# Optimization experiments

Measured on AMD Instinct MI355X. Metric: run time of the kernel, lower is better.

Reference implementation:

```python
import jax, jax.numpy as jnp
import numpy as np

N, E, G = 100000, 1600000, 512
D_IN, D_H, D_OUT = 128, 128, 1
EPS = 1e-5


def _gcn_conv(x, W, b, src, dst, n):
    # PyG GCNConv: h = x @ W, add self-loops, symmetric-normalized sum aggregation, bias after.
    h = x @ W
    loop = jnp.arange(n)
    s = jnp.concatenate([src, loop])
    d = jnp.concatenate([dst, loop])
    deg = jax.ops.segment_sum(jnp.ones(s.shape[0], dtype=h.dtype), d, num_segments=n)
    dinv = jnp.where(deg > 0, jax.lax.rsqrt(deg), 0.0)
    norm = dinv[s] * dinv[d]  # [E+N]
    out = jax.ops.segment_sum(h[s] * norm[:, None], d, num_segments=n)
    return out + b


def _bn(x, g, b, m, v):
    # eval-mode BatchNorm1d
    return (x - m) * jax.lax.rsqrt(v + EPS) * g + b


def setup_inputs() -> dict:
    key = jax.random.key(0)
    ks = jax.random.split(key, 24)
    x = jax.random.normal(ks[0], (N, D_IN), dtype=jnp.float32)
    edge_index = jax.random.randint(ks[1], (2, E), 0, N, dtype=jnp.int64)
    batch = (jnp.arange(N, dtype=jnp.int64) * G) // N  # sorted, all graphs non-empty
    inp = {"x": x, "edge_index": edge_index, "batch": batch}
    dims = [(D_IN, D_H), (D_H, D_H), (D_H, D_H)]
    for i, (din, dout) in enumerate(dims):
        sc = 1.0 / np.sqrt(din)
        inp[f"W{i}"] = jax.random.normal(ks[2 + 4 * i], (din, dout), dtype=jnp.float32) * sc
        inp[f"cb{i}"] = jnp.zeros((dout,), dtype=jnp.float32)
        inp[f"g{i}"] = jnp.ones((dout,), dtype=jnp.float32)
        inp[f"bt{i}"] = jnp.zeros((dout,), dtype=jnp.float32)
        inp[f"m{i}"] = jax.random.normal(ks[3 + 4 * i], (dout,), dtype=jnp.float32) * 0.1
        inp[f"v{i}"] = jax.random.uniform(ks[4 + 4 * i], (dout,), dtype=jnp.float32, minval=0.5, maxval=1.5)
    inp["L1w"] = jax.random.normal(ks[15], (2 * D_H, D_H), dtype=jnp.float32) / np.sqrt(2 * D_H)
    inp["L1b"] = jnp.zeros((D_H,), dtype=jnp.float32)
    inp["L2w"] = jax.random.normal(ks[16], (D_H, D_H // 2), dtype=jnp.float32) / np.sqrt(D_H)
    inp["L2b"] = jnp.zeros((D_H // 2,), dtype=jnp.float32)
    inp["L3w"] = jax.random.normal(ks[17], (D_H // 2, D_OUT), dtype=jnp.float32) / np.sqrt(D_H // 2)
    inp["L3b"] = jnp.zeros((D_OUT,), dtype=jnp.float32)
    return inp


def reference(x, edge_index, batch,
              W0, cb0, g0, bt0, m0, v0,
              W1, cb1, g1, bt1, m1, v1,
              W2, cb2, g2, bt2, m2, v2,
              L1w, L1b, L2w, L2b, L3w, L3b):
    src, dst = edge_index[0], edge_index[1]
    Ws = [W0, W1, W2]
    cbs = [cb0, cb1, cb2]
    bns = [(g0, bt0, m0, v0), (g1, bt1, m1, v1), (g2, bt2, m2, v2)]
    for i in range(3):
        x_prev = x
        x = _gcn_conv(x, Ws[i], cbs[i], src, dst, N)
        x = jax.nn.relu(_bn(x, *bns[i]))
        # dropout is identity in eval mode
        if i > 0:
            x = x + x_prev  # residual (shapes match for i > 0)
    ones = jnp.ones((N,), dtype=x.dtype)
    cnt = jax.ops.segment_sum(ones, batch, num_segments=G)[:, None]
    x_mean = jax.ops.segment_sum(x, batch, num_segments=G) / cnt
    x_max = jax.ops.segment_max(x, batch, num_segments=G)
    h = jnp.concatenate([x_mean, x_max], axis=1)  # [G, 2*D_H]
    h = jax.nn.relu(h @ L1w + L1b)
    h = jax.nn.relu(h @ L2w + L2b)
    return h @ L3w + L3b  # [G, 1]
```

## Files before the change

kernel.cpp:

```cpp
#include <hip/hip_runtime.h>
#include <math.h>

#define DH 128
#define EPSB 1e-5f
#define MAXB 832
#define BCAP 3072

typedef __attribute__((ext_vector_type(8))) short short8;
typedef __attribute__((ext_vector_type(4))) float f32x4;

static __device__ __forceinline__ unsigned short f2bf(float f) {
    unsigned u = __float_as_uint(f);
    u += 0x7fffu + ((u >> 16) & 1u);
    return (unsigned short)(u >> 16);
}
static __device__ __forceinline__ float bf2f(unsigned short h) {
    return __uint_as_float(((unsigned)h) << 16);
}
static __device__ __forceinline__ float blo(unsigned u) { return __uint_as_float(u << 16); }
static __device__ __forceinline__ float bhi(unsigned u) { return __uint_as_float(u & 0xFFFF0000u); }


__launch_bounds__(256)
__global__ void k_bucketA(const int* __restrict__ src, const int* __restrict__ dst,
                          int* __restrict__ gcur, int* __restrict__ bbuf,
                          const int* __restrict__ batch, int* __restrict__ starts,
                          int E, int NB, int chunk, int N, int G)
{
    __shared__ int cnt[MAXB];
    __shared__ int base[MAXB];
    const int t = threadIdx.x;

    for (int i = blockIdx.x * 256 + t; i < N; i += gridDim.x * 256) {
        int b = batch[i];
        if (i == 0) { starts[0] = 0; starts[G] = N; }
        else if (batch[i - 1] != b) starts[b] = i;
    }

    for (int i = t; i < NB; i += 256) cnt[i] = 0;
    __syncthreads();
    const int e0 = blockIdx.x * chunk;
    const int e1 = min(E, e0 + chunk);
    for (int e = e0 + t; e < e1; e += 256)
        atomicAdd(&cnt[dst[e] >> 7], 1);
    __syncthreads();
    for (int i = t; i < NB; i += 256) {
        int c = cnt[i];
        base[i] = (c > 0) ? atomicAdd(&gcur[i], c) : 0;
        cnt[i] = 0;
    }
    __syncthreads();
    for (int e = e0 + t; e < e1; e += 256) {
        int d = dst[e];
        int b = d >> 7;
        int o = base[b] + atomicAdd(&cnt[b], 1);
        if (o < BCAP) bbuf[(size_t)b * BCAP + o] = (src[e] << 7) | (d & 127);
    }
}

__launch_bounds__(1024)
__global__ void k_bgscan(const int* __restrict__ gcur, int* __restrict__ bbase,
                         int* __restrict__ rowptr, int NB, int N, int E)
{
    __shared__ int s[1024];
    int t = threadIdx.x;
    int v = (t < NB) ? min(gcur[t], BCAP) : 0;
    s[t] = v;
    __syncthreads();
    for (int off = 1; off < 1024; off <<= 1) {
        int u = (t >= off) ? s[t - off] : 0;
        __syncthreads();
        s[t] += u;
        __syncthreads();
    }
    if (t < NB) bbase[t] = s[t] - v;
    if (t == 0) rowptr[N] = E;
}

__launch_bounds__(256)
__global__ void k_bfinal(const int* __restrict__ gcur, const int* __restrict__ bbase,
                         const int* __restrict__ bbuf, int* __restrict__ rowptr,
                         float* __restrict__ dinv, int* __restrict__ csr_src, int N)
{
    __shared__ int ebuf[BCAP];
    __shared__ int dcnt[128];
    __shared__ int sp[128];
    const int b = blockIdx.x, t = threadIdx.x;
    const int c = min(gcur[b], BCAP);
    const int base = bbase[b];
    const int* p = bbuf + (size_t)b * BCAP;
    for (int i = t; i < c; i += 256) ebuf[i] = p[i];
    if (t < 128) dcnt[t] = 0;
    __syncthreads();
    for (int i = t; i < c; i += 256) atomicAdd(&dcnt[ebuf[i] & 127], 1);
    __syncthreads();
    if (t < 128) sp[t] = dcnt[t];
    __syncthreads();
    for (int off = 1; off < 128; off <<= 1) {
        int u = (t < 128 && t >= off) ? sp[t - off] : 0;
        __syncthreads();
        if (t < 128) sp[t] += u;
        __syncthreads();
    }
    if (t < 128) {
        sp[t] -= dcnt[t];
        int d = b * 128 + t;
        if (d < N) {
            rowptr[d] = base + sp[t];
            dinv[d] = rsqrtf((float)(dcnt[t] + 1));
        }
        dcnt[t] = 0;
    }
    __syncthreads();
    for (int i = t; i < c; i += 256) {
        int e = ebuf[i];
        int dl = e & 127;
        int o = atomicAdd(&dcnt[dl], 1);
        csr_src[base + sp[dl] + o] = e >> 7;
    }
}


__global__ void k_wfrag(const float* __restrict__ W0, const float* __restrict__ W1,
                        const float* __restrict__ W2, unsigned short* __restrict__ Wf0) {
    int fid = blockIdx.x * 4 + (threadIdx.x >> 6);
    int lane = threadIdx.x & 63;
    int l = fid >> 6;
    int f = fid & 63;
    const float* W = (l == 0) ? W0 : (l == 1) ? W1 : W2;
    unsigned short* Wf = Wf0 + (size_t)l * 32768;
    int nt = f & 3, s = (f >> 2) & 3, p = (f >> 4) & 1, nh = f >> 5;
    int n = nh * 64 + nt * 16 + (lane & 15);
    int kbase = s * 32 + (lane >> 4) * 8;
    unsigned short o[8];
#pragma unroll
    for (int j = 0; j < 8; ++j) {
        float w = W[(size_t)(kbase + j) * DH + n];
        unsigned short h = f2bf(w);
        o[j] = p ? f2bf(w - bf2f(h)) : h;
    }
    unsigned short* d = Wf + (size_t)f * 512 + lane * 8;
    *(ushort4*)d       = make_ushort4(o[0], o[1], o[2], o[3]);
    *(ushort4*)(d + 4) = make_ushort4(o[4], o[5], o[6], o[7]);
}


#define LDA0 132

__launch_bounds__(256)
__global__ void k_gemm0(const float* __restrict__ X,
                        const unsigned short* __restrict__ Wf,
                        const float* __restrict__ dinv,
                        unsigned short* __restrict__ hs, int N)
{
    __shared__ float As[64 * LDA0];

    const int tid  = threadIdx.x;
    const int lane = tid & 63, wave = tid >> 6;
    const int mh = wave >> 1, nh = wave & 1;
    const int rowBase = blockIdx.x * 64;
    const int r15 = lane & 15, quad = lane >> 4;

    {
        const float4* gp = (const float4*)(X + (size_t)rowBase * DH);
#pragma unroll
        for (int it = 0; it < 8; ++it) {
            int idx = it * 256 + tid;
            int grow = idx >> 5, gcol = idx & 31;
            float4 v = make_float4(0.f, 0.f, 0.f, 0.f);
            if (rowBase + grow < N) v = gp[idx];
            *(float4*)(As + grow * LDA0 + gcol * 4) = v;
        }
    }
    __syncthreads();

    f32x4 acc[2][4];
#pragma unroll
    for (int mt = 0; mt < 2; ++mt)
#pragma unroll
        for (int nt = 0; nt < 4; ++nt)
            acc[mt][nt] = (f32x4){0.f, 0.f, 0.f, 0.f};

#pragma unroll
    for (int s = 0; s < 4; ++s) {
        short8 wfh[4], wfl[4];
#pragma unroll
        for (int nt = 0; nt < 4; ++nt) {
            wfh[nt] = *(const short8*)(Wf + ((((nh * 2 + 0) * 4 + s) * 4 + nt) * 512) + lane * 8);
            wfl[nt] = *(const short8*)(Wf + ((((nh * 2 + 1) * 4 + s) * 4 + nt) * 512) + lane * 8);
        }
#pragma unroll
        for (int mt = 0; mt < 2; ++mt) {
            const float* ap = As + (mh * 32 + mt * 16 + r15) * LDA0 + s * 32 + quad * 8;
            short8 ah, al;
#pragma unroll
            for (int j = 0; j < 8; ++j) {
                float v = ap[j];
                unsigned short h = f2bf(v);
                ah[j] = (short)h;
                al[j] = (short)f2bf(v - bf2f(h));
            }
#pragma unroll
            for (int nt = 0; nt < 4; ++nt) {
                acc[mt][nt] = __builtin_amdgcn_mfma_f32_16x16x32_bf16(ah, wfh[nt], acc[mt][nt], 0, 0, 0);
                acc[mt][nt] = __builtin_amdgcn_mfma_f32_16x16x32_bf16(ah, wfl[nt], acc[mt][nt], 0, 0, 0);
                acc[mt][nt] = __builtin_amdgcn_mfma_f32_16x16x32_bf16(al, wfh[nt], acc[mt][nt], 0, 0, 0);
            }
        }
    }

#pragma unroll
    for (int mt = 0; mt < 2; ++mt) {
        int rl = mh * 32 + mt * 16 + quad * 4;
#pragma unroll
        for (int reg = 0; reg < 4; ++reg) {
            int row = rowBase + rl + reg;
            if (row < N) {
                float sc = dinv[row];
#pragma unroll
                for (int nt = 0; nt < 4; ++nt)
                    hs[(size_t)row * DH + nh * 64 + nt * 16 + r15] = f2bf(acc[mt][nt][reg] * sc);
            }
        }
    }
}


#define LDAP 136

__launch_bounds__(256)
__global__ void k_gemm_pl(const unsigned short* __restrict__ Xh,
                          const unsigned short* __restrict__ Xl,
                          const unsigned short* __restrict__ Wf,
                          const float* __restrict__ dinv,
                          unsigned short* __restrict__ hs, int N)
{
    __shared__ unsigned short Ah[64 * LDAP];
    __shared__ unsigned short Al[64 * LDAP];

    const int tid  = threadIdx.x;
    const int lane = tid & 63, wave = tid >> 6;
    const int mh = wave >> 1, nh = wave & 1;
    const int rowBase = blockIdx.x * 64;
    const int r15 = lane & 15, quad = lane >> 4;

    {
        const uint4* gh = (const uint4*)(Xh + (size_t)rowBase * DH);
        const uint4* gl = (const uint4*)(Xl + (size_t)rowBase * DH);
#pragma unroll
        for (int it = 0; it < 4; ++it) {
            int idx = it * 256 + tid;
            int grow = idx >> 4, gcol8 = (idx & 15) * 8;
            uint4 vh = make_uint4(0, 0, 0, 0), vl = make_uint4(0, 0, 0, 0);
            if (rowBase + grow < N) { vh = gh[idx]; vl = gl[idx]; }
            *(uint4*)(Ah + grow * LDAP + gcol8) = vh;
            *(uint4*)(Al + grow * LDAP + gcol8) = vl;
        }
    }
    __syncthreads();

    f32x4 acc[2][4];
#pragma unroll
    for (int mt = 0; mt < 2; ++mt)
#pragma unroll
        for (int nt = 0; nt < 4; ++nt)
            acc[mt][nt] = (f32x4){0.f, 0.f, 0.f, 0.f};

#pragma unroll
    for (int s = 0; s < 4; ++s) {
        short8 wfh[4], wfl[4];
#pragma unroll
        for (int nt = 0; nt < 4; ++nt) {
            wfh[nt] = *(const short8*)(Wf + ((((nh * 2 + 0) * 4 + s) * 4 + nt) * 512) + lane * 8);
            wfl[nt] = *(const short8*)(Wf + ((((nh * 2 + 1) * 4 + s) * 4 + nt) * 512) + lane * 8);
        }
#pragma unroll
        for (int mt = 0; mt < 2; ++mt) {
            int arow = mh * 32 + mt * 16 + r15;
            short8 ah = *(const short8*)(Ah + arow * LDAP + s * 32 + quad * 8);
            short8 al = *(const short8*)(Al + arow * LDAP + s * 32 + quad * 8);
#pragma unroll
            for (int nt = 0; nt < 4; ++nt) {
                acc[mt][nt] = __builtin_amdgcn_mfma_f32_16x16x32_bf16(ah, wfh[nt], acc[mt][nt], 0, 0, 0);
                acc[mt][nt] = __builtin_amdgcn_mfma_f32_16x16x32_bf16(ah, wfl[nt], acc[mt][nt], 0, 0, 0);
                acc[mt][nt] = __builtin_amdgcn_mfma_f32_16x16x32_bf16(al, wfh[nt], acc[mt][nt], 0, 0, 0);
            }
        }
    }

#pragma unroll
    for (int mt = 0; mt < 2; ++mt) {
        int rl = mh * 32 + mt * 16 + quad * 4;
#pragma unroll
        for (int reg = 0; reg < 4; ++reg) {
            int row = rowBase + rl + reg;
            if (row < N) {
                float sc = dinv[row];
#pragma unroll
                for (int nt = 0; nt < 4; ++nt)
                    hs[(size_t)row * DH + nh * 64 + nt * 16 + r15] = f2bf(acc[mt][nt][reg] * sc);
            }
        }
    }
}


__launch_bounds__(256)
__global__ void k_gather(const unsigned short* __restrict__ hs, const int* __restrict__ rowptr,
                         const int* __restrict__ csr_src, const float* __restrict__ dinv,
                         const float* __restrict__ cb, const float* __restrict__ bm,
                         const float* __restrict__ bv, const float* __restrict__ bg,
                         const float* __restrict__ bb,
                         const unsigned short* __restrict__ ph,
                         const unsigned short* __restrict__ pl,
                         unsigned short* __restrict__ oh,
                         unsigned short* __restrict__ ol,
                         int N)
{
    const int node = (blockIdx.x * blockDim.x + threadIdx.x) >> 4;
    const int lh = threadIdx.x & 15;
    if (node >= N) return;
    const int f = lh * 8;
    const int e0 = rowptr[node], e1 = rowptr[node + 1];

    const uint4* hsv = (const uint4*)hs;
    float a[8];
    {
        uint4 sv = hsv[(size_t)node * 16 + lh];
        a[0] = blo(sv.x); a[1] = bhi(sv.x); a[2] = blo(sv.y); a[3] = bhi(sv.y);
        a[4] = blo(sv.z); a[5] = bhi(sv.z); a[6] = blo(sv.w); a[7] = bhi(sv.w);
    }

    for (int base = e0; base < e1; base += 16) {
        int cnt = e1 - base; if (cnt > 16) cnt = 16;
        int idx = (lh < cnt) ? csr_src[base + lh] : 0;
        int i = 0;
        for (; i + 4 <= cnt; i += 4) {
            int s0 = __shfl(idx, i,     16), s1 = __shfl(idx, i + 1, 16);
            int s2 = __shfl(idx, i + 2, 16), s3 = __shfl(idx, i + 3, 16);
            uint4 v0 = hsv[(size_t)s0 * 16 + lh];
            uint4 v1 = hsv[(size_t)s1 * 16 + lh];
            uint4 v2 = hsv[(size_t)s2 * 16 + lh];
            uint4 v3 = hsv[(size_t)s3 * 16 + lh];
            a[0] += (blo(v0.x) + blo(v1.x)) + (blo(v2.x) + blo(v3.x));
            a[1] += (bhi(v0.x) + bhi(v1.x)) + (bhi(v2.x) + bhi(v3.x));
            a[2] += (blo(v0.y) + blo(v1.y)) + (blo(v2.y) + blo(v3.y));
            a[3] += (bhi(v0.y) + bhi(v1.y)) + (bhi(v2.y) + bhi(v3.y));
            a[4] += (blo(v0.z) + blo(v1.z)) + (blo(v2.z) + blo(v3.z));
            a[5] += (bhi(v0.z) + bhi(v1.z)) + (bhi(v2.z) + bhi(v3.z));
            a[6] += (blo(v0.w) + blo(v1.w)) + (blo(v2.w) + blo(v3.w));
            a[7] += (bhi(v0.w) + bhi(v1.w)) + (bhi(v2.w) + bhi(v3.w));
        }
        for (; i < cnt; ++i) {
            int s = __shfl(idx, i, 16);
            uint4 v = hsv[(size_t)s * 16 + lh];
            a[0] += blo(v.x); a[1] += bhi(v.x); a[2] += blo(v.y); a[3] += bhi(v.y);
            a[4] += blo(v.z); a[5] += bhi(v.z); a[6] += blo(v.w); a[7] += bhi(v.w);
        }
    }

    const float sc = dinv[node];
    float cbv[8], bmv[8], bvv[8], bgv[8], bbv[8];
    *(float4*)cbv = *(const float4*)(cb + f); *(float4*)(cbv + 4) = *(const float4*)(cb + f + 4);
    *(float4*)bmv = *(const float4*)(bm + f); *(float4*)(bmv + 4) = *(const float4*)(bm + f + 4);
    *(float4*)bvv = *(const float4*)(bv + f); *(float4*)(bvv + 4) = *(const float4*)(bv + f + 4);
    *(float4*)bgv = *(const float4*)(bg + f); *(float4*)(bgv + 4) = *(const float4*)(bg + f + 4);
    *(float4*)bbv = *(const float4*)(bb + f); *(float4*)(bbv + 4) = *(const float4*)(bb + f + 4);

    float o[8];
#pragma unroll
    for (int j = 0; j < 8; ++j) {
        float v = (a[j] * sc + cbv[j] - bmv[j]) * rsqrtf(bvv[j] + EPSB) * bgv[j] + bbv[j];
        o[j] = fmaxf(v, 0.f);
    }
    if (ph) {
        uint4 hv = *(const uint4*)(ph + (size_t)node * DH + f);
        uint4 lv = *(const uint4*)(pl + (size_t)node * DH + f);
        o[0] += blo(hv.x) + blo(lv.x); o[1] += bhi(hv.x) + bhi(lv.x);
        o[2] += blo(hv.y) + blo(lv.y); o[3] += bhi(hv.y) + bhi(lv.y);
        o[4] += blo(hv.z) + blo(lv.z); o[5] += bhi(hv.z) + bhi(lv.z);
        o[6] += blo(hv.w) + blo(lv.w); o[7] += bhi(hv.w) + bhi(lv.w);
    }
    unsigned hw[4], lw[4];
#pragma unroll
    for (int p = 0; p < 4; ++p) {
        unsigned short hA = f2bf(o[2 * p]), hB = f2bf(o[2 * p + 1]);
        hw[p] = (unsigned)hA | ((unsigned)hB << 16);
        lw[p] = (unsigned)f2bf(o[2 * p] - bf2f(hA)) |
                ((unsigned)f2bf(o[2 * p + 1] - bf2f(hB)) << 16);
    }
    *(uint4*)(oh + (size_t)node * DH + f) = make_uint4(hw[0], hw[1], hw[2], hw[3]);
    *(uint4*)(ol + (size_t)node * DH + f) = make_uint4(lw[0], lw[1], lw[2], lw[3]);
}


__launch_bounds__(256)
__global__ void k_pool_mlp(const unsigned short* __restrict__ xh,
                           const unsigned short* __restrict__ xl,
                           const int* __restrict__ starts,
                           const float* __restrict__ L1w, const float* __restrict__ L1b,
                           const float* __restrict__ L2w, const float* __restrict__ L2b,
                           const float* __restrict__ L3w, const float* __restrict__ L3b,
                           float* __restrict__ out)
{
    int g = blockIdx.x, t = threadIdx.x;
    int s0 = starts[g], s1 = starts[g + 1];
    const int rg = t >> 6;
    const int tc = t & 63;
    const int fc = tc * 2;

    float sA = 0.f, sB = 0.f;
    float mA = -INFINITY, mB = -INFINITY;
    for (int i = s0 + rg; i < s1; i += 4) {
        unsigned hv = *(const unsigned*)(xh + (size_t)i * DH + fc);
        unsigned lv = *(const unsigned*)(xl + (size_t)i * DH + fc);
        float vA = blo(hv) + blo(lv);
        float vB = bhi(hv) + bhi(lv);
        sA += vA; sB += vB;
        mA = fmaxf(mA, vA); mB = fmaxf(mB, vB);
    }

    __shared__ float ps[4][128];
    __shared__ float pm[4][128];
    ps[rg][fc] = sA; ps[rg][fc + 1] = sB;
    pm[rg][fc] = mA; pm[rg][fc + 1] = mB;
    __syncthreads();

    __shared__ float h[256];
    if (rg == 0) {
        float inv = 1.f / (float)(s1 - s0);
#pragma unroll
        for (int j = 0; j < 2; ++j) {
            int fi = fc + j;
            h[fi] = ((ps[0][fi] + ps[1][fi]) + (ps[2][fi] + ps[3][fi])) * inv;
            h[128 + fi] = fmaxf(fmaxf(pm[0][fi], pm[1][fi]), fmaxf(pm[2][fi], pm[3][fi]));
        }
    }
    __syncthreads();

    __shared__ float h1[128];
    if (t < 128) {
        float a = L1b[t];
        for (int k = 0; k < 256; ++k) a += h[k] * L1w[k * DH + t];
        h1[t] = fmaxf(a, 0.f);
    }
    __syncthreads();

    __shared__ float h2[64];
    if (t < 64) {
        float a2 = L2b[t];
        for (int k = 0; k < 128; ++k) a2 += h1[k] * L2w[k * 64 + t];
        h2[t] = fmaxf(a2, 0.f);
    }
    __syncthreads();

    if (t < 64) {
        float p = h2[t] * L3w[t];
#pragma unroll
        for (int off = 32; off > 0; off >>= 1) p += __shfl_down(p, off, 64);
        if (t == 0) out[g] = p + L3b[0];
    }
}


static inline char* align16(char* p) {
    return (char*)(((uintptr_t)p + 15) & ~(uintptr_t)15);
}

extern "C" void kernel_launch(void* const* d_in, const int* in_sizes, int n_in,
                              void* d_out, int out_size, void* d_ws, size_t ws_size,
                              hipStream_t stream)
{
    const float* x     = (const float*)d_in[0];
    const int*   ei    = (const int*)d_in[1];
    const int*   batch = (const int*)d_in[2];
    const int N = in_sizes[0] / DH;
    const int E = in_sizes[1] / 2;
    const int G = out_size;
    const int* src = ei;
    const int* dst = ei + E;

    const float* W[3]  = {(const float*)d_in[3],  (const float*)d_in[9],  (const float*)d_in[15]};
    const float* cb[3] = {(const float*)d_in[4],  (const float*)d_in[10], (const float*)d_in[16]};
    const float* bg[3] = {(const float*)d_in[5],  (const float*)d_in[11], (const float*)d_in[17]};
    const float* bt[3] = {(const float*)d_in[6],  (const float*)d_in[12], (const float*)d_in[18]};
    const float* bm[3] = {(const float*)d_in[7],  (const float*)d_in[13], (const float*)d_in[19]};
    const float* bv[3] = {(const float*)d_in[8],  (const float*)d_in[14], (const float*)d_in[20]};
    const float* L1w = (const float*)d_in[21]; const float* L1b = (const float*)d_in[22];
    const float* L2w = (const float*)d_in[23]; const float* L2b = (const float*)d_in[24];
    const float* L3w = (const float*)d_in[25]; const float* L3b = (const float*)d_in[26];

    char* wsp = (char*)d_ws;
    size_t planeB = (size_t)N * DH * sizeof(unsigned short);
    unsigned short* HS  = (unsigned short*)wsp; wsp += planeB;
    unsigned short* AH  = (unsigned short*)wsp; wsp += planeB;
    unsigned short* AL  = (unsigned short*)wsp; wsp += planeB;
    unsigned short* BH  = (unsigned short*)wsp; wsp += planeB;
    unsigned short* BL  = (unsigned short*)wsp; wsp += planeB;
    unsigned short* Wfrag = (unsigned short*)wsp; wsp += 3 * 65536;
    float* dinv   = (float*)wsp; wsp += (size_t)N * sizeof(float);
    int*   rowptr = (int*)wsp;   wsp = align16(wsp + (size_t)(N + 1) * sizeof(int));
    int*   csr_src= (int*)wsp;   wsp += (size_t)E * sizeof(int);
    int*   starts = (int*)wsp;   wsp = align16(wsp + (size_t)(G + 1) * sizeof(int));
    int*   gcur   = (int*)wsp;   wsp = align16(wsp + (size_t)MAXB * sizeof(int));
    int*   bbase  = (int*)wsp;   wsp = align16(wsp + (size_t)MAXB * sizeof(int));
    int*   bbuf   = (int*)wsp;   wsp += (size_t)MAXB * BCAP * sizeof(int);

    const int NB = (N + 127) >> 7;
    const int nblkA = 512;
    const int chunk = (E + nblkA - 1) / nblkA;

    hipMemsetAsync(gcur, 0, (size_t)NB * sizeof(int), stream);
    k_bucketA<<<nblkA, 256, 0, stream>>>(src, dst, gcur, bbuf, batch, starts,
                                         E, NB, chunk, N, G);
    k_bgscan <<<1, 1024, 0, stream>>>(gcur, bbase, rowptr, NB, N, E);
    k_bfinal <<<NB, 256, 0, stream>>>(gcur, bbase, bbuf, rowptr, dinv, csr_src, N);
    k_wfrag  <<<48, 256, 0, stream>>>(W[0], W[1], W[2], Wfrag);

    int gemmGrid = (N + 63) / 64;
    int gathGrid = ((size_t)N * 16 + 255) / 256;

    k_gemm0<<<gemmGrid, 256, 0, stream>>>(x, Wfrag, dinv, HS, N);
    k_gather<<<gathGrid, 256, 0, stream>>>(HS, rowptr, csr_src, dinv,
                                           cb[0], bm[0], bv[0], bg[0], bt[0],
                                           nullptr, nullptr, AH, AL, N);
    k_gemm_pl<<<gemmGrid, 256, 0, stream>>>(AH, AL, Wfrag + 32768, dinv, HS, N);
    k_gather<<<gathGrid, 256, 0, stream>>>(HS, rowptr, csr_src, dinv,
                                           cb[1], bm[1], bv[1], bg[1], bt[1],
                                           AH, AL, BH, BL, N);
    k_gemm_pl<<<gemmGrid, 256, 0, stream>>>(BH, BL, Wfrag + 65536, dinv, HS, N);
    k_gather<<<gathGrid, 256, 0, stream>>>(HS, rowptr, csr_src, dinv,
                                           cb[2], bm[2], bv[2], bg[2], bt[2],
                                           BH, BL, AH, AL, N);

    k_pool_mlp<<<G, 256, 0, stream>>>(AH, AL, starts, L1w, L1b, L2w, L2b, L3w, L3b,
                                      (float*)d_out);
}
```

Measured before the change: 507.4 us.

## Fuse neighbor gather with next-layer GEMM and drop CSR scan kernel

Each layer's gather/BN/ReLU/residual step now also runs the next layer's bf16 split-precision MFMA GEMM on its 16-node tile held in shared memory. This removes the separate GEMM kernels and the hi/lo bf16 activation planes, which are replaced by fp32 feature buffers. The CSR is built in place inside the padded per-bucket buffers, with int2 row ranges, so the global scan kernel is gone. The weight-fragment packing is folded into the bucketing launch as extra blocks. The trade-offs are a small GEMM tile per block with repeated weight-fragment loads, more fp32 feature traffic, and a smaller bucket capacity that could overflow on skewed degree distributions.

```diff
diff --git a/kernel.cpp b/kernel.cpp
--- a/kernel.cpp
+++ b/kernel.cpp
@@ -4,7 +4,8 @@
 #define DH 128
 #define EPSB 1e-5f
 #define MAXB 832
-#define BCAP 3072
+#define BCAP 2560
+#define LDAP 136
 
 typedef __attribute__((ext_vector_type(8))) short short8;
 typedef __attribute__((ext_vector_type(4))) float f32x4;
@@ -25,13 +26,38 @@
 __global__ void k_bucketA(const int* __restrict__ src, const int* __restrict__ dst,
                           int* __restrict__ gcur, int* __restrict__ bbuf,
                           const int* __restrict__ batch, int* __restrict__ starts,
+                          const float* __restrict__ W0, const float* __restrict__ W1,
+                          const float* __restrict__ W2, unsigned short* __restrict__ Wf0,
                           int E, int NB, int chunk, int N, int G)
 {
+    const int t = threadIdx.x;
+
+    if (blockIdx.x >= 512) {
+        int fid = (blockIdx.x - 512) * 4 + (t >> 6);
+        int lane = t & 63;
+        int l = fid >> 6, f = fid & 63;
+        const float* W = (l == 0) ? W0 : (l == 1) ? W1 : W2;
+        unsigned short* Wf = Wf0 + (size_t)l * 32768;
+        int nt = f & 3, s = (f >> 2) & 3, p = (f >> 4) & 1, nh = f >> 5;
+        int n = nh * 64 + nt * 16 + (lane & 15);
+        int kbase = s * 32 + (lane >> 4) * 8;
+        unsigned short o[8];
+#pragma unroll
+        for (int j = 0; j < 8; ++j) {
+            float w = W[(size_t)(kbase + j) * DH + n];
+            unsigned short h = f2bf(w);
+            o[j] = p ? f2bf(w - bf2f(h)) : h;
+        }
+        unsigned short* d = Wf + (size_t)f * 512 + lane * 8;
+        *(ushort4*)d       = make_ushort4(o[0], o[1], o[2], o[3]);
+        *(ushort4*)(d + 4) = make_ushort4(o[4], o[5], o[6], o[7]);
+        return;
+    }
+
     __shared__ int cnt[MAXB];
     __shared__ int base[MAXB];
-    const int t = threadIdx.x;
-
-    for (int i = blockIdx.x * 256 + t; i < N; i += gridDim.x * 256) {
+
+    for (int i = blockIdx.x * 256 + t; i < N; i += 512 * 256) {
         int b = batch[i];
         if (i == 0) { starts[0] = 0; starts[G] = N; }
         else if (batch[i - 1] != b) starts[b] = i;
@@ -58,37 +84,18 @@
     }
 }
 
-__launch_bounds__(1024)
-__global__ void k_bgscan(const int* __restrict__ gcur, int* __restrict__ bbase,
-                         int* __restrict__ rowptr, int NB, int N, int E)
-{
-    __shared__ int s[1024];
-    int t = threadIdx.x;
-    int v = (t < NB) ? min(gcur[t], BCAP) : 0;
-    s[t] = v;
-    __syncthreads();
-    for (int off = 1; off < 1024; off <<= 1) {
-        int u = (t >= off) ? s[t - off] : 0;
-        __syncthreads();
-        s[t] += u;
-        __syncthreads();
-    }
-    if (t < NB) bbase[t] = s[t] - v;
-    if (t == 0) rowptr[N] = E;
-}
 
 __launch_bounds__(256)
-__global__ void k_bfinal(const int* __restrict__ gcur, const int* __restrict__ bbase,
-                         const int* __restrict__ bbuf, int* __restrict__ rowptr,
-                         float* __restrict__ dinv, int* __restrict__ csr_src, int N)
+__global__ void k_bfinal(const int* __restrict__ gcur, int* __restrict__ bbuf,
+                         int2* __restrict__ rowinfo, float* __restrict__ dinv, int N)
 {
     __shared__ int ebuf[BCAP];
     __shared__ int dcnt[128];
     __shared__ int sp[128];
     const int b = blockIdx.x, t = threadIdx.x;
     const int c = min(gcur[b], BCAP);
-    const int base = bbase[b];
-    const int* p = bbuf + (size_t)b * BCAP;
+    const int base = b * BCAP;
+    int* p = bbuf + base;
     for (int i = t; i < c; i += 256) ebuf[i] = p[i];
     if (t < 128) dcnt[t] = 0;
     __syncthreads();
@@ -106,7 +113,7 @@
         sp[t] -= dcnt[t];
         int d = b * 128 + t;
         if (d < N) {
-            rowptr[d] = base + sp[t];
+            rowinfo[d] = make_int2(base + sp[t], base + sp[t] + dcnt[t]);
             dinv[d] = rsqrtf((float)(dcnt[t] + 1));
         }
         dcnt[t] = 0;
@@ -116,32 +123,8 @@
         int e = ebuf[i];
         int dl = e & 127;
         int o = atomicAdd(&dcnt[dl], 1);
-        csr_src[base + sp[dl] + o] = e >> 7;
-    }
-}
-
-
-__global__ void k_wfrag(const float* __restrict__ W0, const float* __restrict__ W1,
-                        const float* __restrict__ W2, unsigned short* __restrict__ Wf0) {
-    int fid = blockIdx.x * 4 + (threadIdx.x >> 6);
-    int lane = threadIdx.x & 63;
-    int l = fid >> 6;
-    int f = fid & 63;
-    const float* W = (l == 0) ? W0 : (l == 1) ? W1 : W2;
-    unsigned short* Wf = Wf0 + (size_t)l * 32768;
-    int nt = f & 3, s = (f >> 2) & 3, p = (f >> 4) & 1, nh = f >> 5;
-    int n = nh * 64 + nt * 16 + (lane & 15);
-    int kbase = s * 32 + (lane >> 4) * 8;
-    unsigned short o[8];
-#pragma unroll
-    for (int j = 0; j < 8; ++j) {
-        float w = W[(size_t)(kbase + j) * DH + n];
-        unsigned short h = f2bf(w);
-        o[j] = p ? f2bf(w - bf2f(h)) : h;
-    }
-    unsigned short* d = Wf + (size_t)f * 512 + lane * 8;
-    *(ushort4*)d       = make_ushort4(o[0], o[1], o[2], o[3]);
-    *(ushort4*)(d + 4) = make_ushort4(o[4], o[5], o[6], o[7]);
+        p[sp[dl] + o] = e >> 7;
+    }
 }
 
 
@@ -226,102 +209,160 @@
 }
 
 
-#define LDAP 136
-
 __launch_bounds__(256)
-__global__ void k_gemm_pl(const unsigned short* __restrict__ Xh,
-                          const unsigned short* __restrict__ Xl,
-                          const unsigned short* __restrict__ Wf,
-                          const float* __restrict__ dinv,
-                          unsigned short* __restrict__ hs, int N)
-{
-    __shared__ unsigned short Ah[64 * LDAP];
-    __shared__ unsigned short Al[64 * LDAP];
-
-    const int tid  = threadIdx.x;
+__global__ void k_gather_mm(const unsigned short* __restrict__ hs,
+                            const int2* __restrict__ rowinfo,
+                            const int* __restrict__ csr_src,
+                            const float* __restrict__ dinv,
+                            const float* __restrict__ cb, const float* __restrict__ bm,
+                            const float* __restrict__ bv, const float* __restrict__ bg,
+                            const float* __restrict__ bb,
+                            const float* __restrict__ prev,
+                            float* __restrict__ feat,
+                            const unsigned short* __restrict__ Wf,
+                            unsigned short* __restrict__ hs_next,
+                            int N)
+{
+    __shared__ unsigned short Ah[16 * LDAP];
+    __shared__ unsigned short Al[16 * LDAP];
+
+    const int tid = threadIdx.x;
+    const int nb = tid >> 4, lh = tid & 15;
+    const int nodeBase = blockIdx.x * 16;
+    const int node = nodeBase + nb;
+    const int f = lh * 8;
+
+    if (node < N) {
+        int2 ri = rowinfo[node];
+        const uint4* hsv = (const uint4*)hs;
+        float a[8];
+        {
+            uint4 sv = hsv[(size_t)node * 16 + lh];
+            a[0] = blo(sv.x); a[1] = bhi(sv.x); a[2] = blo(sv.y); a[3] = bhi(sv.y);
+            a[4] = blo(sv.z); a[5] = bhi(sv.z); a[6] = blo(sv.w); a[7] = bhi(sv.w);
+        }
+        for (int base = ri.x; base < ri.y; base += 16) {
+            int cnt = ri.y - base; if (cnt > 16) cnt = 16;
+            int idx = (lh < cnt) ? csr_src[base + lh] : 0;
+            int i = 0;
+            for (; i + 4 <= cnt; i += 4) {
+                int s0 = __shfl(idx, i,     16), s1 = __shfl(idx, i + 1, 16);
+                int s2 = __shfl(idx, i + 2, 16), s3 = __shfl(idx, i + 3, 16);
+                uint4 v0 = hsv[(size_t)s0 * 16 + lh];
+                uint4 v1 = hsv[(size_t)s1 * 16 + lh];
+                uint4 v2 = hsv[(size_t)s2 * 16 + lh];
+                uint4 v3 = hsv[(size_t)s3 * 16 + lh];
+                a[0] += (blo(v0.x) + blo(v1.x)) + (blo(v2.x) + blo(v3.x));
+                a[1] += (bhi(v0.x) + bhi(v1.x)) + (bhi(v2.x) + bhi(v3.x));
+                a[2] += (blo(v0.y) + blo(v1.y)) + (blo(v2.y) + blo(v3.y));
+                a[3] += (bhi(v0.y) + bhi(v1.y)) + (bhi(v2.y) + bhi(v3.y));
+                a[4] += (blo(v0.z) + blo(v1.z)) + (blo(v2.z) + blo(v3.z));
+                a[5] += (bhi(v0.z) + bhi(v1.z)) + (bhi(v2.z) + bhi(v3.z));
+                a[6] += (blo(v0.w) + blo(v1.w)) + (blo(v2.w) + blo(v3.w));
+                a[7] += (bhi(v0.w) + bhi(v1.w)) + (bhi(v2.w) + bhi(v3.w));
+            }
+            for (; i < cnt; ++i) {
+                int s = __shfl(idx, i, 16);
+                uint4 v = hsv[(size_t)s * 16 + lh];
+                a[0] += blo(v.x); a[1] += bhi(v.x); a[2] += blo(v.y); a[3] += bhi(v.y);
+                a[4] += blo(v.z); a[5] += bhi(v.z); a[6] += blo(v.w); a[7] += bhi(v.w);
+            }
+        }
+
+        const float sc = dinv[node];
+        float cbv[8], bmv[8], bvv[8], bgv[8], bbv[8];
+        *(float4*)cbv = *(const float4*)(cb + f); *(float4*)(cbv + 4) = *(const float4*)(cb + f + 4);
+        *(float4*)bmv = *(const float4*)(bm + f); *(float4*)(bmv + 4) = *(const float4*)(bm + f + 4);
+        *(float4*)bvv = *(const float4*)(bv + f); *(float4*)(bvv + 4) = *(const float4*)(bv + f + 4);
+        *(float4*)bgv = *(const float4*)(bg + f); *(float4*)(bgv + 4) = *(const float4*)(bg + f + 4);
+        *(float4*)bbv = *(const float4*)(bb + f); *(float4*)(bbv + 4) = *(const float4*)(bb + f + 4);
+
+        float o[8];
+#pragma unroll
+        for (int j = 0; j < 8; ++j) {
+            float v = (a[j] * sc + cbv[j] - bmv[j]) * rsqrtf(bvv[j] + EPSB) * bgv[j] + bbv[j];
+            o[j] = fmaxf(v, 0.f);
+        }
+        if (prev) {
+            float4 p0 = *(const float4*)(prev + (size_t)node * DH + f);
+            float4 p1 = *(const float4*)(prev + (size_t)node * DH + f + 4);
+            o[0] += p0.x; o[1] += p0.y; o[2] += p0.z; o[3] += p0.w;
+            o[4] += p1.x; o[5] += p1.y; o[6] += p1.z; o[7] += p1.w;
+        }
+        *(float4*)(feat + (size_t)node * DH + f)     = make_float4(o[0], o[1], o[2], o[3]);
+        *(float4*)(feat + (size_t)node * DH + f + 4) = make_float4(o[4], o[5], o[6], o[7]);
+
+        unsigned short hA[8], lA[8];
+#pragma unroll
+        for (int j = 0; j < 8; ++j) {
+            unsigned short h = f2bf(o[j]);
+            hA[j] = h; lA[j] = f2bf(o[j] - bf2f(h));
+        }
+        *(ushort4*)(Ah + nb * LDAP + f)     = make_ushort4(hA[0], hA[1], hA[2], hA[3]);
+        *(ushort4*)(Ah + nb * LDAP + f + 4) = make_ushort4(hA[4], hA[5], hA[6], hA[7]);
+        *(ushort4*)(Al + nb * LDAP + f)     = make_ushort4(lA[0], lA[1], lA[2], lA[3]);
+        *(ushort4*)(Al + nb * LDAP + f + 4) = make_ushort4(lA[4], lA[5], lA[6], lA[7]);
+    }
+    __syncthreads();
+
     const int lane = tid & 63, wave = tid >> 6;
-    const int mh = wave >> 1, nh = wave & 1;
-    const int rowBase = blockIdx.x * 64;
     const int r15 = lane & 15, quad = lane >> 4;
 
-    {
-        const uint4* gh = (const uint4*)(Xh + (size_t)rowBase * DH);
-        const uint4* gl = (const uint4*)(Xl + (size_t)rowBase * DH);
-#pragma unroll
-        for (int it = 0; it < 4; ++it) {
-            int idx = it * 256 + tid;
-            int grow = idx >> 4, gcol8 = (idx & 15) * 8;
-            uint4 vh = make_uint4(0, 0, 0, 0), vl = make_uint4(0, 0, 0, 0);
-            if (rowBase + grow < N) { vh = gh[idx]; vl = gl[idx]; }
-            *(uint4*)(Ah + grow * LDAP + gcol8) = vh;
-            *(uint4*)(Al + grow * LDAP + gcol8) = vl;
-        }
-    }
-    __syncthreads();
-
-    f32x4 acc[2][4];
-#pragma unroll
-    for (int mt = 0; mt < 2; ++mt)
-#pragma unroll
-        for (int nt = 0; nt < 4; ++nt)
-            acc[mt][nt] = (f32x4){0.f, 0.f, 0.f, 0.f};
+    f32x4 acc[2];
+    acc[0] = (f32x4){0.f, 0.f, 0.f, 0.f};
+    acc[1] = (f32x4){0.f, 0.f, 0.f, 0.f};
 
 #pragma unroll
     for (int s = 0; s < 4; ++s) {
-        short8 wfh[4], wfl[4];
-#pragma unroll
-        for (int nt = 0; nt < 4; ++nt) {
-            wfh[nt] = *(const short8*)(Wf + ((((nh * 2 + 0) * 4 + s) * 4 + nt) * 512) + lane * 8);
-            wfl[nt] = *(const short8*)(Wf + ((((nh * 2 + 1) * 4 + s) * 4 + nt) * 512) + lane * 8);
-        }
-#pragma unroll
-        for (int mt = 0; mt < 2; ++mt) {
-            int arow = mh * 32 + mt * 16 + r15;
-            short8 ah = *(const short8*)(Ah + arow * LDAP + s * 32 + quad * 8);
-            short8 al = *(const short8*)(Al + arow * LDAP + s * 32 + quad * 8);
-#pragma unroll
-            for (int nt = 0; nt < 4; ++nt) {
-                acc[mt][nt] = __builtin_amdgcn_mfma_f32_16x16x32_bf16(ah, wfh[nt], acc[mt][nt], 0, 0, 0);
-                acc[mt][nt] = __builtin_amdgcn_mfma_f32_16x16x32_bf16(ah, wfl[nt], acc[mt][nt], 0, 0, 0);
-                acc[mt][nt] = __builtin_amdgcn_mfma_f32_16x16x32_bf16(al, wfh[nt], acc[mt][nt], 0, 0, 0);
-            }
-        }
-    }
-
-#pragma unroll
-    for (int mt = 0; mt < 2; ++mt) {
-        int rl = mh * 32 + mt * 16 + quad * 4;
+        short8 ah = *(const short8*)(Ah + r15 * LDAP + s * 32 + quad * 8);
+        short8 al = *(const short8*)(Al + r15 * LDAP + s * 32 + quad * 8);
+#pragma unroll
+        for (int j = 0; j < 2; ++j) {
+            int ntg = wave * 2 + j;
+            int nh = ntg >> 2, nt = ntg & 3;
+            short8 wh = *(const short8*)(Wf + ((((nh * 2 + 0) * 4 + s) * 4 + nt) * 512) + lane * 8);
+            short8 wl = *(const short8*)(Wf + ((((nh * 2 + 1) * 4 + s) * 4 + nt) * 512) + lane * 8);
+            acc[j] = __builtin_amdgcn_mfma_f32_16x16x32_bf16(ah, wh, acc[j], 0, 0, 0);
+            acc[j] = __builtin_amdgcn_mfma_f32_16x16x32_bf16(ah, wl, acc[j], 0, 0, 0);
+            acc[j] = __builtin_amdgcn_mfma_f32_16x16x32_bf16(al, wh, acc[j], 0, 0, 0);
+        }
+    }
+
+    float dv[4];
+#pragma unroll
+    for (int reg = 0; reg < 4; ++reg) {
+        int row = nodeBase + quad * 4 + reg;
+        dv[reg] = (row < N) ? dinv[row] : 0.f;
+    }
+#pragma unroll
+    for (int j = 0; j < 2; ++j) {
+        int col = (wave * 2 + j) * 16 + r15;
 #pragma unroll
         for (int reg = 0; reg < 4; ++reg) {
-            int row = rowBase + rl + reg;
-            if (row < N) {
-                float sc = dinv[row];
-#pragma unroll
-                for (int nt = 0; nt < 4; ++nt)
-                    hs[(size_t)row * DH + nh * 64 + nt * 16 + r15] = f2bf(acc[mt][nt][reg] * sc);
-            }
+            int row = nodeBase + quad * 4 + reg;
+            if (row < N)
+                hs_next[(size_t)row * DH + col] = f2bf(acc[j][reg] * dv[reg]);
         }
     }
 }
 
 
 __launch_bounds__(256)
-__global__ void k_gather(const unsigned short* __restrict__ hs, const int* __restrict__ rowptr,
-                         const int* __restrict__ csr_src, const float* __restrict__ dinv,
-                         const float* __restrict__ cb, const float* __restrict__ bm,
-                         const float* __restrict__ bv, const float* __restrict__ bg,
-                         const float* __restrict__ bb,
-                         const unsigned short* __restrict__ ph,
-                         const unsigned short* __restrict__ pl,
-                         unsigned short* __restrict__ oh,
-                         unsigned short* __restrict__ ol,
-                         int N)
+__global__ void k_gather_fin(const unsigned short* __restrict__ hs,
+                             const int2* __restrict__ rowinfo,
+                             const int* __restrict__ csr_src,
+                             const float* __restrict__ dinv,
+                             const float* __restrict__ cb, const float* __restrict__ bm,
+                             const float* __restrict__ bv, const float* __restrict__ bg,
+                             const float* __restrict__ bb,
+                             const float* __restrict__ prev,
+                             float* __restrict__ feat, int N)
 {
     const int node = (blockIdx.x * blockDim.x + threadIdx.x) >> 4;
     const int lh = threadIdx.x & 15;
     if (node >= N) return;
     const int f = lh * 8;
-    const int e0 = rowptr[node], e1 = rowptr[node + 1];
+    int2 ri = rowinfo[node];
 
     const uint4* hsv = (const uint4*)hs;
     float a[8];
@@ -330,9 +371,8 @@
         a[0] = blo(sv.x); a[1] = bhi(sv.x); a[2] = blo(sv.y); a[3] = bhi(sv.y);
         a[4] = blo(sv.z); a[5] = bhi(sv.z); a[6] = blo(sv.w); a[7] = bhi(sv.w);
     }
-
-    for (int base = e0; base < e1; base += 16) {
-        int cnt = e1 - base; if (cnt > 16) cnt = 16;
+    for (int base = ri.x; base < ri.y; base += 16) {
+        int cnt = ri.y - base; if (cnt > 16) cnt = 16;
         int idx = (lh < cnt) ? csr_src[base + lh] : 0;
         int i = 0;
         for (; i + 4 <= cnt; i += 4) {
@@ -367,37 +407,24 @@
     *(float4*)bgv = *(const float4*)(bg + f); *(float4*)(bgv + 4) = *(const float4*)(bg + f + 4);
     *(float4*)bbv = *(const float4*)(bb + f); *(float4*)(bbv + 4) = *(const float4*)(bb + f + 4);
 
+    float4 p0 = *(const float4*)(prev + (size_t)node * DH + f);
+    float4 p1 = *(const float4*)(prev + (size_t)node * DH + f + 4);
     float o[8];
 #pragma unroll
     for (int j = 0; j < 8; ++j) {
         float v = (a[j] * sc + cbv[j] - bmv[j]) * rsqrtf(bvv[j] + EPSB) * bgv[j] + bbv[j];
         o[j] = fmaxf(v, 0.f);
     }
-    if (ph) {
-        uint4 hv = *(const uint4*)(ph + (size_t)node * DH + f);
-        uint4 lv = *(const uint4*)(pl + (size_t)node * DH + f);
-        o[0] += blo(hv.x) + blo(lv.x); o[1] += bhi(hv.x) + bhi(lv.x);
-        o[2] += blo(hv.y) + blo(lv.y); o[3] += bhi(hv.y) + bhi(lv.y);
-        o[4] += blo(hv.z) + blo(lv.z); o[5] += bhi(hv.z) + bhi(lv.z);
-        o[6] += blo(hv.w) + blo(lv.w); o[7] += bhi(hv.w) + bhi(lv.w);
-    }
-    unsigned hw[4], lw[4];
-#pragma unroll
-    for (int p = 0; p < 4; ++p) {
-        unsigned short hA = f2bf(o[2 * p]), hB = f2bf(o[2 * p + 1]);
-        hw[p] = (unsigned)hA | ((unsigned)hB << 16);
-        lw[p] = (unsigned)f2bf(o[2 * p] - bf2f(hA)) |
-                ((unsigned)f2bf(o[2 * p + 1] - bf2f(hB)) << 16);
-    }
-    *(uint4*)(oh + (size_t)node * DH + f) = make_uint4(hw[0], hw[1], hw[2], hw[3]);
-    *(uint4*)(ol + (size_t)node * DH + f) = make_uint4(lw[0], lw[1], lw[2], lw[3]);
+    o[0] += p0.x; o[1] += p0.y; o[2] += p0.z; o[3] += p0.w;
+    o[4] += p1.x; o[5] += p1.y; o[6] += p1.z; o[7] += p1.w;
+
+    *(float4*)(feat + (size_t)node * DH + f)     = make_float4(o[0], o[1], o[2], o[3]);
+    *(float4*)(feat + (size_t)node * DH + f + 4) = make_float4(o[4], o[5], o[6], o[7]);
 }
 
 
 __launch_bounds__(256)
-__global__ void k_pool_mlp(const unsigned short* __restrict__ xh,
-                           const unsigned short* __restrict__ xl,
-                           const int* __restrict__ starts,
+__global__ void k_pool_mlp(const float* __restrict__ x, const int* __restrict__ starts,
                            const float* __restrict__ L1w, const float* __restrict__ L1b,
                            const float* __restrict__ L2w, const float* __restrict__ L2b,
                            const float* __restrict__ L3w, const float* __restrict__ L3b,
@@ -412,12 +439,9 @@
     float sA = 0.f, sB = 0.f;
     float mA = -INFINITY, mB = -INFINITY;
     for (int i = s0 + rg; i < s1; i += 4) {
-        unsigned hv = *(const unsigned*)(xh + (size_t)i * DH + fc);
-        unsigned lv = *(const unsigned*)(xl + (size_t)i * DH + fc);
-        float vA = blo(hv) + blo(lv);
-        float vB = bhi(hv) + bhi(lv);
-        sA += vA; sB += vB;
-        mA = fmaxf(mA, vA); mB = fmaxf(mB, vB);
+        float2 v = *(const float2*)(x + (size_t)i * DH + fc);
+        sA += v.x; sB += v.y;
+        mA = fmaxf(mA, v.x); mB = fmaxf(mB, v.y);
     }
 
     __shared__ float ps[4][128];
@@ -491,48 +515,44 @@
     const float* L3w = (const float*)d_in[25]; const float* L3b = (const float*)d_in[26];
 
     char* wsp = (char*)d_ws;
-    size_t planeB = (size_t)N * DH * sizeof(unsigned short);
-    unsigned short* HS  = (unsigned short*)wsp; wsp += planeB;
-    unsigned short* AH  = (unsigned short*)wsp; wsp += planeB;
-    unsigned short* AL  = (unsigned short*)wsp; wsp += planeB;
-    unsigned short* BH  = (unsigned short*)wsp; wsp += planeB;
-    unsigned short* BL  = (unsigned short*)wsp; wsp += planeB;
+    size_t featB = (size_t)N * DH * sizeof(float);
+    size_t hsB   = (size_t)N * DH * sizeof(unsigned short);
+    float* F_A = (float*)wsp; wsp += featB;
+    float* F_B = (float*)wsp; wsp += featB;
+    unsigned short* HS0 = (unsigned short*)F_B;
+    unsigned short* HS1 = (unsigned short*)wsp; wsp += hsB;
+    unsigned short* HS2 = (unsigned short*)wsp; wsp += hsB;
     unsigned short* Wfrag = (unsigned short*)wsp; wsp += 3 * 65536;
-    float* dinv   = (float*)wsp; wsp += (size_t)N * sizeof(float);
-    int*   rowptr = (int*)wsp;   wsp = align16(wsp + (size_t)(N + 1) * sizeof(int));
-    int*   csr_src= (int*)wsp;   wsp += (size_t)E * sizeof(int);
-    int*   starts = (int*)wsp;   wsp = align16(wsp + (size_t)(G + 1) * sizeof(int));
-    int*   gcur   = (int*)wsp;   wsp = align16(wsp + (size_t)MAXB * sizeof(int));
-    int*   bbase  = (int*)wsp;   wsp = align16(wsp + (size_t)MAXB * sizeof(int));
-    int*   bbuf   = (int*)wsp;   wsp += (size_t)MAXB * BCAP * sizeof(int);
+    int2*  rowinfo = (int2*)wsp;  wsp += (size_t)N * sizeof(int2);
+    float* dinv    = (float*)wsp; wsp += (size_t)N * sizeof(float);
+    int*   starts  = (int*)wsp;   wsp = align16(wsp + (size_t)(G + 1) * sizeof(int));
+    int*   gcur    = (int*)wsp;   wsp = align16(wsp + (size_t)MAXB * sizeof(int));
+    int*   bbuf    = (int*)wsp;   wsp += (size_t)MAXB * BCAP * sizeof(int);
 
     const int NB = (N + 127) >> 7;
     const int nblkA = 512;
     const int chunk = (E + nblkA - 1) / nblkA;
 
     hipMemsetAsync(gcur, 0, (size_t)NB * sizeof(int), stream);
-    k_bucketA<<<nblkA, 256, 0, stream>>>(src, dst, gcur, bbuf, batch, starts,
-                                         E, NB, chunk, N, G);
-    k_bgscan <<<1, 1024, 0, stream>>>(gcur, bbase, rowptr, NB, N, E);
-    k_bfinal <<<NB, 256, 0, stream>>>(gcur, bbase, bbuf, rowptr, dinv, csr_src, N);
-    k_wfrag  <<<48, 256, 0, stream>>>(W[0], W[1], W[2], Wfrag);
+    k_bucketA<<<nblkA + 48, 256, 0, stream>>>(src, dst, gcur, bbuf, batch, starts,
+                                              W[0], W[1], W[2], Wfrag,
+                                              E, NB, chunk, N, G);
+    k_bfinal <<<NB, 256, 0, stream>>>(gcur, bbuf, rowinfo, dinv, N);
 
     int gemmGrid = (N + 63) / 64;
     int gathGrid = ((size_t)N * 16 + 255) / 256;
 
-    k_gemm0<<<gemmGrid, 256, 0, stream>>>(x, Wfrag, dinv, HS, N);
-    k_gather<<<gathGrid, 256, 0, stream>>>(HS, rowptr, csr_src, dinv,
-                                           cb[0], bm[0], bv[0], bg[0], bt[0],
-                                           nullptr, nullptr, AH, AL, N);
-    k_gemm_pl<<<gemmGrid, 256, 0, stream>>>(AH, AL, Wfrag + 32768, dinv, HS, N);
-    k_gather<<<gathGrid, 256, 0, stream>>>(HS, rowptr, csr_src, dinv,
-                                           cb[1], bm[1], bv[1], bg[1], bt[1],
-                                           AH, AL, BH, BL, N);
-    k_gemm_pl<<<gemmGrid, 256, 0, stream>>>(BH, BL, Wfrag + 65536, dinv, HS, N);
-    k_gather<<<gathGrid, 256, 0, stream>>>(HS, rowptr, csr_src, dinv,
-                                           cb[2], bm[2], bv[2], bg[2], bt[2],
-                                           BH, BL, AH, AL, N);
-
-    k_pool_mlp<<<G, 256, 0, stream>>>(AH, AL, starts, L1w, L1b, L2w, L2b, L3w, L3b,
+    k_gemm0<<<gemmGrid, 256, 0, stream>>>(x, Wfrag, dinv, HS0, N);
+    k_gather_mm<<<gathGrid, 256, 0, stream>>>(HS0, rowinfo, bbuf, dinv,
+                                              cb[0], bm[0], bv[0], bg[0], bt[0],
+                                              nullptr, F_A, Wfrag + 32768, HS1, N);
+    k_gather_mm<<<gathGrid, 256, 0, stream>>>(HS1, rowinfo, bbuf, dinv,
+                                              cb[1], bm[1], bv[1], bg[1], bt[1],
+                                              F_A, F_B, Wfrag + 65536, HS2, N);
+    k_gather_fin<<<gathGrid, 256, 0, stream>>>(HS2, rowinfo, bbuf, dinv,
+                                               cb[2], bm[2], bv[2], bg[2], bt[2],
+                                               F_B, F_B, N);
+
+    k_pool_mlp<<<G, 256, 0, stream>>>(F_B, starts, L1w, L1b, L2w, L2b, L3w, L3b,
                                       (float*)d_out);
 }
```

After: 486.7 us. -4.1%, faster.
